# Kernel tuning notes

Hardware: AMD Instinct MI355X
Metric: run time of the kernel (lower is better)

Reference implementation:

```python
import jax, jax.numpy as jnp
import numpy as np

N_NODES = 50000
N_PAIRS = 200000
HID1 = 256
HID2 = 32


def gcn_conv(x, src, dst, W, b, n):
    # PyG GCNConv: project, add self-loops, sym-normalize, scatter-add to dst.
    sl = jnp.arange(n, dtype=src.dtype)
    s = jnp.concatenate([src, sl])
    d = jnp.concatenate([dst, sl])
    deg = jnp.zeros((n,), x.dtype).at[d].add(1.0)
    dinv = jax.lax.rsqrt(deg)  # deg >= 1 due to self-loops
    xw = x @ W  # [n, out]
    msg = xw[s] * (dinv[s] * dinv[d])[:, None]  # [E+n, out]
    out = jax.ops.segment_sum(msg, d, num_segments=n)
    return out + b


def setup_inputs() -> dict:
    key = jax.random.key(0)
    ks = jax.random.split(key, 16)
    inp = {
        "x": jax.random.randint(ks[0], (N_NODES,), 0, N_NODES),
        "edge1": jax.random.randint(ks[1], (2, 1600000), 0, N_NODES),
        "pos": jax.random.randint(ks[2], (N_PAIRS, 2), 0, N_NODES),
        "idx": jax.random.randint(ks[3], (N_PAIRS,), 0, N_PAIRS),
        "ei2": jax.random.randint(ks[4], (2, 1600000), 0, N_PAIRS),
        "emb_table": jax.random.normal(ks[5], (N_NODES + 1, HID1), jnp.float32) * 0.02,
        "W1": jax.random.normal(ks[6], (HID1, HID2), jnp.float32) * (1.0 / np.sqrt(HID1)),
        "b1": jnp.zeros((HID2,), jnp.float32),
        "W2a": jax.random.normal(ks[7], (HID2, HID2), jnp.float32) * (1.0 / np.sqrt(HID2)),
        "b2a": jnp.zeros((HID2,), jnp.float32),
        "W2b": jax.random.normal(ks[8], (HID2, HID2), jnp.float32) * (1.0 / np.sqrt(HID2)),
        "b2b": jnp.zeros((HID2,), jnp.float32),
        "Wp": jax.random.normal(ks[9], (HID2, 1), jnp.float32) * (1.0 / np.sqrt(HID2)),
        "bp": jnp.zeros((1,), jnp.float32),
    }
    return inp


def reference(x, edge1, pos, idx, ei2, emb_table, W1, b1, W2a, b2a, W2b, b2b, Wp, bp):
    # eval mode: all Dropouts are identity; no LayerNorm/GraphNorm (default flags False)
    h = emb_table[x]  # [N, HID1] embedding lookup (squeeze is no-op for 1D ids)
    # conv1s: single GCNConv HID1 -> HID2 + ReLU
    h = jax.nn.relu(gcn_conv(h, edge1[0], edge1[1], W1, b1, N_NODES))
    # pairwise gather-multiply over pos
    h = h[pos[:, 0]] * h[pos[:, 1]]  # [M, HID2]
    # conv2s / conv2s_r on the pair graph (edge2 = ei2, edge2_r = flipped)
    h = (jax.nn.relu(gcn_conv(h, ei2[0], ei2[1], W2a, b2a, N_PAIRS))
         + jax.nn.relu(gcn_conv(h, ei2[1], ei2[0], W2b, b2b, N_PAIRS)))
    # gather by idx, then multiply consecutive (even, odd) rows
    h = h[idx]  # [2Q, HID2]
    h = h[0::2] * h[1::2]  # [Q, HID2]
    return h @ Wp + bp  # [Q, 1]
```

## Files before the change

kernel.cpp:

```cpp
#include <hip/hip_runtime.h>
#include <hip/hip_fp16.h>
#include <math.h>


#define SL     256
#define SLOG   8
#define CAP1   8960
#define CAP2   2432
#define SHIFT1 17
#define SHIFT2 18
#define BCH    8192
#define BT     1024
#define EPT    8
#define MAXSL2 1024
#define PB     64
#define EROW   264

typedef short bf16x8 __attribute__((ext_vector_type(8)));
typedef float f32x4 __attribute__((ext_vector_type(4)));

static __device__ __forceinline__ unsigned short f2bf(float f) {
    union { float f; unsigned u; } v;
    v.f = f;
    unsigned r = v.u + 0x7FFF + ((v.u >> 16) & 1);
    return (unsigned short)(r >> 16);
}
static __device__ __forceinline__ float bf2f(unsigned short h) {
    return __uint_as_float(((unsigned)h) << 16);
}
static __device__ __forceinline__ float bflo(unsigned u) { return __uint_as_float(u << 16); }
static __device__ __forceinline__ float bfhi(unsigned u) { return __uint_as_float(u & 0xFFFF0000u); }

static __device__ __forceinline__ float4 bfacc(float4 a, uint2 w) {
    a.x += bflo(w.x);
    a.y += bfhi(w.x);
    a.z += bflo(w.y);
    a.w += bfhi(w.y);
    return a;
}
static __device__ __forceinline__ float4 hacc(float4 a, uint2 w) {
    float2 f0 = __half22float2(*(__half2*)&w.x);
    float2 f1 = __half22float2(*(__half2*)&w.y);
    a.x += f0.x;
    a.y += f0.y;
    a.z += f1.x;
    a.w += f1.y;
    return a;
}
static __device__ __forceinline__ float4 h2f4(uint2 w) {
    float2 f0 = __half22float2(*(__half2*)&w.x);
    float2 f1 = __half22float2(*(__half2*)&w.y);
    float4 r = {f0.x, f0.y, f1.x, f1.y};
    return r;
}
static __device__ __forceinline__ uint2 f42h(float4 f) {
    __half2 h0 = __floats2half2_rn(f.x, f.y);
    __half2 h1 = __floats2half2_rn(f.z, f.w);
    uint2 r = {*(unsigned*)&h0, *(unsigned*)&h1};
    return r;
}

__global__ __launch_bounds__(256) void k_init(int* __restrict__ bumpF,
                                              int* __restrict__ bumpR,
                                              int* __restrict__ bump1,
                                              int NS2, int NS1) {
    int i = blockIdx.x * 256 + threadIdx.x;
    if (i < NS2) {
        bumpF[i] = i * CAP2;
        bumpR[i] = i * CAP2;
    }
    if (i < NS1) bump1[i] = i * CAP1;
}

__global__ __launch_bounds__(BT) void k_build(const int* __restrict__ s2,
                                              const int* __restrict__ d2,
                                              const int* __restrict__ s1,
                                              const int* __restrict__ d1,
                                              int* bumpF, int* bumpR, int* bump1,
                                              int* __restrict__ bktF,
                                              int* __restrict__ bktR,
                                              int* __restrict__ bkt1,
                                              const float* __restrict__ W1,
                                              const float* __restrict__ W2a,
                                              const float* __restrict__ W2b,
                                              unsigned short* __restrict__ Wbhi,
                                              unsigned short* __restrict__ Wblo,
                                              unsigned short* __restrict__ W2ah,
                                              unsigned short* __restrict__ W2al,
                                              unsigned short* __restrict__ W2bh,
                                              unsigned short* __restrict__ W2bl,
                                              int E2, int E1, int NS2, int NS1,
                                              int NB2, int NB1) {
    __shared__ int stag[BCH];
    __shared__ int lbF[MAXSL2 + 1];
    __shared__ int lbR[MAXSL2 + 1];
    __shared__ int bgF[MAXSL2], bgR[MAXSL2];
    __shared__ int wsum[BT / 64];
    int tid = threadIdx.x, bid = blockIdx.x;
    int lane = tid & 63, wid = tid >> 6;

    auto exscan = [&](int v) -> int {
        int sc = v;
#pragma unroll
        for (int d = 1; d < 64; d <<= 1) {
            int t = __shfl_up(sc, d, 64);
            if (lane >= d) sc += t;
        }
        if (lane == 63) wsum[wid] = sc;
        __syncthreads();
        int woff = 0;
        for (int w2 = 0; w2 < wid; w2++) woff += wsum[w2];
        __syncthreads();
        return woff + sc - v;
    };

    if (bid < NB2) {
        if (tid < NS2) { lbF[tid] = 0; lbR[tid] = 0; }
        __syncthreads();
        int eb = bid * BCH;
        int n = E2 - eb; if (n > BCH) n = BCH;
        int sv[EPT], dv[EPT], ofF[EPT], ofR[EPT];
#pragma unroll
        for (int k = 0; k < EPT; k++) {
            int i = k * BT + tid;
            if (i < n) {
                sv[k] = s2[eb + i];
                dv[k] = d2[eb + i];
                ofF[k] = atomicAdd(&lbF[dv[k] >> SLOG], 1);
                ofR[k] = atomicAdd(&lbR[sv[k] >> SLOG], 1);
            }
        }
        __syncthreads();
        int cF = (tid < NS2) ? lbF[tid] : 0;
        int cR = (tid < NS2) ? lbR[tid] : 0;
        int preF = exscan(cF);
        int preR = exscan(cR);
        if (tid < NS2) {
            lbF[tid] = preF;
            lbR[tid] = preR;
            if (tid == NS2 - 1) {
                lbF[NS2] = preF + cF;
                lbR[NS2] = preR + cR;
            }
            bgF[tid] = cF ? atomicAdd(&bumpF[tid], cF) : 0;
            bgR[tid] = cR ? atomicAdd(&bumpR[tid], cR) : 0;
        }
        __syncthreads();
#pragma unroll
        for (int k = 0; k < EPT; k++) {
            int i = k * BT + tid;
            if (i < n) {
                int sf = dv[k] >> SLOG;
                stag[lbF[sf] + ofF[k]] = ((dv[k] & (SL - 1)) << SHIFT2) | sv[k];
            }
        }
        __syncthreads();
        for (int i = tid; i < n; i += BT) {
            int lo = 0, hi = NS2;
            while (hi - lo > 1) {
                int mid = (lo + hi) >> 1;
                if (lbF[mid] <= i) lo = mid; else hi = mid;
            }
            int gp = bgF[lo] + (i - lbF[lo]);
            if (gp < (lo + 1) * CAP2) bktF[gp] = stag[i];
        }
        __syncthreads();
#pragma unroll
        for (int k = 0; k < EPT; k++) {
            int i = k * BT + tid;
            if (i < n) {
                int sr = sv[k] >> SLOG;
                stag[lbR[sr] + ofR[k]] = ((sv[k] & (SL - 1)) << SHIFT2) | dv[k];
            }
        }
        __syncthreads();
        for (int i = tid; i < n; i += BT) {
            int lo = 0, hi = NS2;
            while (hi - lo > 1) {
                int mid = (lo + hi) >> 1;
                if (lbR[mid] <= i) lo = mid; else hi = mid;
            }
            int gp = bgR[lo] + (i - lbR[lo]);
            if (gp < (lo + 1) * CAP2) bktR[gp] = stag[i];
        }
    } else if (bid < NB2 + NB1) {
        if (tid < NS1) lbF[tid] = 0;
        __syncthreads();
        int eb = (bid - NB2) * BCH;
        int n = E1 - eb; if (n > BCH) n = BCH;
        int sv[EPT], dv[EPT], of[EPT];
#pragma unroll
        for (int k = 0; k < EPT; k++) {
            int i = k * BT + tid;
            if (i < n) {
                sv[k] = s1[eb + i];
                dv[k] = d1[eb + i];
                of[k] = atomicAdd(&lbF[dv[k] >> SLOG], 1);
            }
        }
        __syncthreads();
        int c = (tid < NS1) ? lbF[tid] : 0;
        int pre = exscan(c);
        if (tid < NS1) {
            lbF[tid] = pre;
            if (tid == NS1 - 1) lbF[NS1] = pre + c;
            bgF[tid] = c ? atomicAdd(&bump1[tid], c) : 0;
        }
        __syncthreads();
#pragma unroll
        for (int k = 0; k < EPT; k++) {
            int i = k * BT + tid;
            if (i < n) {
                int sf = dv[k] >> SLOG;
                stag[lbF[sf] + of[k]] = ((dv[k] & (SL - 1)) << SHIFT1) | sv[k];
            }
        }
        __syncthreads();
        for (int i = tid; i < n; i += BT) {
            int lo = 0, hi = NS1;
            while (hi - lo > 1) {
                int mid = (lo + hi) >> 1;
                if (lbF[mid] <= i) lo = mid; else hi = mid;
            }
            int gp = bgF[lo] + (i - lbF[lo]);
            if (gp < (lo + 1) * CAP1) bkt1[gp] = stag[i];
        }
    } else {
        int i = (bid - NB2 - NB1) * BT + tid;
        if (i < 8192) {
            int k = i >> 5, c = i & 31;
            float w = W1[i];
            unsigned short hi = f2bf(w);
            unsigned short lo = f2bf(w - bf2f(hi));
            Wbhi[c * 256 + k] = hi;
            Wblo[c * 256 + k] = lo;
        }
        if (i < 1024) {
            int k = i >> 5, c = i & 31;
            float wa = W2a[i], wb = W2b[i];
            unsigned short ha = f2bf(wa);
            unsigned short hb = f2bf(wb);
            W2ah[c * 32 + k] = ha;
            W2al[c * 32 + k] = f2bf(wa - bf2f(ha));
            W2bh[c * 32 + k] = hb;
            W2bl[c * 32 + k] = f2bf(wb - bf2f(hb));
        }
    }
}

__global__ __launch_bounds__(256) void k_sort2(int* __restrict__ bktF, const int* __restrict__ bumpF,
                                               float* __restrict__ dinvF, int* __restrict__ begF,
                                               int* __restrict__ cntF,
                                               int* __restrict__ bktR, const int* __restrict__ bumpR,
                                               float* __restrict__ dinvR, int* __restrict__ begR,
                                               int* __restrict__ cntR,
                                               int NS2, int NP) {
    __shared__ int sorted[CAP2];
    __shared__ int hist[SL], cursor[SL];
    __shared__ int wsum[4];
    int bid = blockIdx.x;
    int s;
    int* bkt;
    const int* bump;
    float* dinv;
    int* beg;
    int* cntA;
    if (bid < NS2) {
        s = bid;
        bkt = bktF; bump = bumpF; dinv = dinvF; beg = begF; cntA = cntF;
    } else {
        s = bid - NS2;
        bkt = bktR; bump = bumpR; dinv = dinvR; beg = begR; cntA = cntR;
    }
    int tid = threadIdx.x;
    hist[tid] = 0;
    __syncthreads();
    int cnt = bump[s] - s * CAP2;
    if (cnt > CAP2) cnt = CAP2;
    int* b = bkt + (size_t)s * CAP2;
    for (int i = tid; i < cnt; i += 256) atomicAdd(&hist[b[i] >> SHIFT2], 1);
    __syncthreads();
    int c = hist[tid];
    int sc = c;
    int lane = tid & 63, wid = tid >> 6;
#pragma unroll
    for (int d = 1; d < 64; d <<= 1) {
        int t = __shfl_up(sc, d, 64);
        if (lane >= d) sc += t;
    }
    if (lane == 63) wsum[wid] = sc;
    __syncthreads();
    int woff = 0;
    for (int w = 0; w < wid; w++) woff += wsum[w];
    int pre = woff + sc - c;
    cursor[tid] = pre;
    int v = s * SL + tid;
    if (v < NP) {
        dinv[v] = 1.f / sqrtf((float)c + 1.f);
        beg[v] = s * CAP2 + pre;
        cntA[v] = c;
    }
    __syncthreads();
    for (int i = tid; i < cnt; i += 256) {
        int pair = b[i];
        int dl = pair >> SHIFT2;
        int p = atomicAdd(&cursor[dl], 1);
        sorted[p] = pair & ((1 << SHIFT2) - 1);
    }
    __syncthreads();
    for (int i = tid; i < cnt; i += 256) b[i] = sorted[i];
}

__global__ __launch_bounds__(1024) void k_sort1(int* __restrict__ bkt1, const int* __restrict__ bump1,
                                                float* __restrict__ dinv1, int* __restrict__ beg1,
                                                int* __restrict__ cnt1, int N1) {
    __shared__ int sorted[CAP1];
    __shared__ int hist[SL], cursor[SL];
    __shared__ int wsum[4];
    int tid = threadIdx.x, s = blockIdx.x;
    if (tid < SL) hist[tid] = 0;
    __syncthreads();
    int cnt = bump1[s] - s * CAP1;
    if (cnt > CAP1) cnt = CAP1;
    int* b = bkt1 + (size_t)s * CAP1;
    for (int i = tid; i < cnt; i += 1024) atomicAdd(&hist[b[i] >> SHIFT1], 1);
    __syncthreads();
    int c = 0, sc = 0;
    int lane = tid & 63, wid = tid >> 6;
    if (tid < SL) {
        c = hist[tid];
        sc = c;
#pragma unroll
        for (int d = 1; d < 64; d <<= 1) {
            int t = __shfl_up(sc, d, 64);
            if (lane >= d) sc += t;
        }
        if (lane == 63) wsum[wid] = sc;
    }
    __syncthreads();
    if (tid < SL) {
        int woff = 0;
        for (int w = 0; w < wid; w++) woff += wsum[w];
        int pre = woff + sc - c;
        cursor[tid] = pre;
        int v = s * SL + tid;
        if (v < N1) {
            dinv1[v] = 1.f / sqrtf((float)c + 1.f);
            beg1[v] = s * CAP1 + pre;
            cnt1[v] = c;
        }
    }
    __syncthreads();
    for (int i = tid; i < cnt; i += 1024) {
        int pair = b[i];
        int dl = pair >> SHIFT1;
        int p = atomicAdd(&cursor[dl], 1);
        sorted[p] = pair & ((1 << SHIFT1) - 1);
    }
    __syncthreads();
    for (int i = tid; i < cnt; i += 1024) b[i] = sorted[i];
}

__global__ __launch_bounds__(256) void k_xw1(const int* __restrict__ x,
                                             const float* __restrict__ emb,
                                             const unsigned short* __restrict__ Wbhi,
                                             const unsigned short* __restrict__ Wblo,
                                             const float* __restrict__ dinv1,
                                             __half* __restrict__ y1, int N) {
    __shared__ unsigned short sEhi[32 * EROW];
    __shared__ unsigned short sElo[32 * EROW];
    int tid = threadIdx.x;
    int lane = tid & 63, wv = tid >> 6;
    int r0 = blockIdx.x * 32;
    const float4* emb4 = (const float4*)emb;
#pragma unroll
    for (int p = 0; p < 8; p++) {
        int row = p * 4 + wv;
        int r = r0 + row;
        int xr = x[(r < N) ? r : 0];
        float4 e = emb4[(size_t)xr * 64 + lane];
        unsigned short h0 = f2bf(e.x), h1 = f2bf(e.y), h2 = f2bf(e.z), h3 = f2bf(e.w);
        ushort4 hi = {h0, h1, h2, h3};
        ushort4 lo = {f2bf(e.x - bf2f(h0)), f2bf(e.y - bf2f(h1)),
                      f2bf(e.z - bf2f(h2)), f2bf(e.w - bf2f(h3))};
        *(ushort4*)&sEhi[row * EROW + lane * 4] = hi;
        *(ushort4*)&sElo[row * EROW + lane * 4] = lo;
    }
    __syncthreads();
    int col = lane & 15, quad = lane >> 4;
    int rowtile = wv >> 1, ntile = wv & 1;
    f32x4 acc = {0.f, 0.f, 0.f, 0.f};
    const unsigned short* arow_hi = &sEhi[(rowtile * 16 + col) * EROW + quad * 8];
    const unsigned short* arow_lo = &sElo[(rowtile * 16 + col) * EROW + quad * 8];
    const unsigned short* bh = Wbhi + (ntile * 16 + col) * 256 + quad * 8;
    const unsigned short* bl = Wblo + (ntile * 16 + col) * 256 + quad * 8;
#pragma unroll
    for (int kb = 0; kb < 256; kb += 32) {
        bf16x8 ahi = *(const bf16x8*)(arow_hi + kb);
        bf16x8 alo = *(const bf16x8*)(arow_lo + kb);
        bf16x8 bhv = *(const bf16x8*)(bh + kb);
        bf16x8 blv = *(const bf16x8*)(bl + kb);
        acc = __builtin_amdgcn_mfma_f32_16x16x32_bf16(ahi, bhv, acc, 0, 0, 0);
        acc = __builtin_amdgcn_mfma_f32_16x16x32_bf16(alo, bhv, acc, 0, 0, 0);
        acc = __builtin_amdgcn_mfma_f32_16x16x32_bf16(ahi, blv, acc, 0, 0, 0);
    }
#pragma unroll
    for (int reg = 0; reg < 4; reg++) {
        int grow = r0 + rowtile * 16 + quad * 4 + reg;
        if (grow < N) {
            float dv = dinv1[grow];
            y1[grow * 32 + ntile * 16 + col] = __float2half(acc[reg] * dv);
        }
    }
}

static __device__ __forceinline__ float4 gcn_sum_h(const int* __restrict__ adj, int bg, int end,
                                                   const uint2* __restrict__ y2, int q,
                                                   float4 acc) {
    float4 a1 = {0.f, 0.f, 0.f, 0.f};
    int i = bg;
    for (; i + 4 <= end; i += 4) {
        int u0 = adj[i], u1 = adj[i + 1], u2 = adj[i + 2], u3 = adj[i + 3];
        uint2 w0 = y2[u0 * 8 + q];
        uint2 w1 = y2[u1 * 8 + q];
        uint2 w2 = y2[u2 * 8 + q];
        uint2 w3 = y2[u3 * 8 + q];
        acc = hacc(acc, w0);
        a1 = hacc(a1, w1);
        acc = hacc(acc, w2);
        a1 = hacc(a1, w3);
    }
    for (; i < end; i++) acc = hacc(acc, y2[adj[i] * 8 + q]);
    acc.x += a1.x;
    acc.y += a1.y;
    acc.z += a1.z;
    acc.w += a1.w;
    return acc;
}

static __device__ __forceinline__ float4 gcn_sum_bf(const int* __restrict__ adj, int bg, int end,
                                                    const uint2* __restrict__ y2, int q,
                                                    float4 acc) {
    float4 a1 = {0.f, 0.f, 0.f, 0.f};
    int i = bg;
    for (; i + 4 <= end; i += 4) {
        int u0 = adj[i], u1 = adj[i + 1], u2 = adj[i + 2], u3 = adj[i + 3];
        uint2 w0 = y2[u0 * 8 + q];
        uint2 w1 = y2[u1 * 8 + q];
        uint2 w2 = y2[u2 * 8 + q];
        uint2 w3 = y2[u3 * 8 + q];
        acc = bfacc(acc, w0);
        a1 = bfacc(a1, w1);
        acc = bfacc(acc, w2);
        a1 = bfacc(a1, w3);
    }
    for (; i < end; i++) acc = bfacc(acc, y2[adj[i] * 8 + q]);
    acc.x += a1.x;
    acc.y += a1.y;
    acc.z += a1.z;
    acc.w += a1.w;
    return acc;
}

__global__ __launch_bounds__(256) void k_gath1(const int* __restrict__ adj,
                                               const int* __restrict__ beg,
                                               const int* __restrict__ cntA,
                                               const float* __restrict__ dinv,
                                               const __half* __restrict__ y1,
                                               __half* __restrict__ out1, int N) {
    int gid = blockIdx.x * 256 + threadIdx.x;
    int v = gid >> 3, q = gid & 7;
    if (v >= N) return;
    int bg = beg[v];
    int end = bg + cntA[v];
    float dv = dinv[v];
    const uint2* y2 = (const uint2*)y1;
    float4 acc = {0.f, 0.f, 0.f, 0.f};
    acc = hacc(acc, y2[v * 8 + q]);
    acc = gcn_sum_h(adj, bg, end, y2, q, acc);
    acc.x *= dv;
    acc.y *= dv;
    acc.z *= dv;
    acc.w *= dv;
    ((uint2*)out1)[v * 8 + q] = f42h(acc);
}

__global__ __launch_bounds__(256) void k_gathF(const int* __restrict__ adjF,
                                               const int* __restrict__ begF,
                                               const int* __restrict__ cntF,
                                               const float* __restrict__ dinvF,
                                               const unsigned short* __restrict__ ya,
                                               __half* __restrict__ o2a, int N) {
    int gid = blockIdx.x * 256 + threadIdx.x;
    int v = gid >> 3, q = gid & 7;
    if (v >= N) return;
    float dvF = dinvF[v];
    const uint2* ya2 = (const uint2*)ya;
    float4 aF = {0.f, 0.f, 0.f, 0.f};
    aF = bfacc(aF, ya2[v * 8 + q]);
    int bgF = begF[v];
    aF = gcn_sum_bf(adjF, bgF, bgF + cntF[v], ya2, q, aF);
    aF.x *= dvF;
    aF.y *= dvF;
    aF.z *= dvF;
    aF.w *= dvF;
    ((uint2*)o2a)[v * 8 + q] = f42h(aF);
}

__global__ __launch_bounds__(256) void k_gathR(const int* __restrict__ adjR,
                                               const int* __restrict__ begR,
                                               const int* __restrict__ cntR,
                                               const float* __restrict__ dinvR,
                                               const unsigned short* __restrict__ yb,
                                               const __half* __restrict__ o2a,
                                               const float* __restrict__ b2a,
                                               const float* __restrict__ b2b,
                                               __half* __restrict__ h3, int N) {
    int gid = blockIdx.x * 256 + threadIdx.x;
    int v = gid >> 3, q = gid & 7;
    if (v >= N) return;
    float dvR = dinvR[v];
    const uint2* yb2 = (const uint2*)yb;
    float4 aR = {0.f, 0.f, 0.f, 0.f};
    aR = bfacc(aR, yb2[v * 8 + q]);
    int bgR = begR[v];
    aR = gcn_sum_bf(adjR, bgR, bgR + cntR[v], yb2, q, aR);
    float4 oa = h2f4(((const uint2*)o2a)[v * 8 + q]);
    float4 ba = ((const float4*)b2a)[q];
    float4 bb = ((const float4*)b2b)[q];
    float4 h;
    h.x = fmaxf(oa.x + ba.x, 0.f) + fmaxf(fmaf(aR.x, dvR, bb.x), 0.f);
    h.y = fmaxf(oa.y + ba.y, 0.f) + fmaxf(fmaf(aR.y, dvR, bb.y), 0.f);
    h.z = fmaxf(oa.z + ba.z, 0.f) + fmaxf(fmaf(aR.z, dvR, bb.z), 0.f);
    h.w = fmaxf(oa.w + ba.w, 0.f) + fmaxf(fmaf(aR.w, dvR, bb.w), 0.f);
    ((uint2*)h3)[v * 8 + q] = f42h(h);
}

__global__ __launch_bounds__(256) void k_xw2(const int* __restrict__ pos,
                                             const __half* __restrict__ out1,
                                             const float* __restrict__ b1,
                                             const unsigned short* __restrict__ W2ah,
                                             const unsigned short* __restrict__ W2al,
                                             const unsigned short* __restrict__ W2bh,
                                             const unsigned short* __restrict__ W2bl,
                                             const float* __restrict__ dinvF,
                                             const float* __restrict__ dinvR,
                                             unsigned short* __restrict__ ya,
                                             unsigned short* __restrict__ yb,
                                             int NP) {
    __shared__ unsigned short sHhi[PB * 32];
    __shared__ unsigned short sHlo[PB * 32];
    __shared__ int sPos[PB * 2];
    int tid = threadIdx.x;
    int p0 = blockIdx.x * PB;
    if (tid < PB * 2) {
        int gi = p0 * 2 + tid;
        sPos[tid] = (gi < NP * 2) ? pos[gi] : 0;
    }
    __syncthreads();
    const uint2* o12 = (const uint2*)out1;
    int q = tid & 7;
    float4 bq = ((const float4*)b1)[q];
#pragma unroll
    for (int half = 0; half < 2; half++) {
        int p = half * 32 + (tid >> 3);
        int ra = sPos[2 * p] * 8, rb = sPos[2 * p + 1] * 8;
        float4 ea = h2f4(o12[ra + q]);
        float4 eb = h2f4(o12[rb + q]);
        float4 h;
        h.x = fmaxf(ea.x + bq.x, 0.f) * fmaxf(eb.x + bq.x, 0.f);
        h.y = fmaxf(ea.y + bq.y, 0.f) * fmaxf(eb.y + bq.y, 0.f);
        h.z = fmaxf(ea.z + bq.z, 0.f) * fmaxf(eb.z + bq.z, 0.f);
        h.w = fmaxf(ea.w + bq.w, 0.f) * fmaxf(eb.w + bq.w, 0.f);
        unsigned short h0 = f2bf(h.x), h1 = f2bf(h.y), h2 = f2bf(h.z), h3 = f2bf(h.w);
        ushort4 hi = {h0, h1, h2, h3};
        ushort4 lo = {f2bf(h.x - bf2f(h0)), f2bf(h.y - bf2f(h1)),
                      f2bf(h.z - bf2f(h2)), f2bf(h.w - bf2f(h3))};
        *(ushort4*)&sHhi[p * 32 + q * 4] = hi;
        *(ushort4*)&sHlo[p * 32 + q * 4] = lo;
    }
    __syncthreads();
    int lane = tid & 63, wv = tid >> 6;
    int col = lane & 15, quad = lane >> 4;
    bf16x8 ahi = *(const bf16x8*)&sHhi[(wv * 16 + col) * 32 + quad * 8];
    bf16x8 alo = *(const bf16x8*)&sHlo[(wv * 16 + col) * 32 + quad * 8];
    f32x4 accA[2], accB[2];
#pragma unroll
    for (int nt = 0; nt < 2; nt++) {
        int off = (nt * 16 + col) * 32 + quad * 8;
        bf16x8 bah = *(const bf16x8*)(W2ah + off);
        bf16x8 bal = *(const bf16x8*)(W2al + off);
        bf16x8 bbh = *(const bf16x8*)(W2bh + off);
        bf16x8 bbl = *(const bf16x8*)(W2bl + off);
        f32x4 z = {0.f, 0.f, 0.f, 0.f};
        f32x4 a = __builtin_amdgcn_mfma_f32_16x16x32_bf16(ahi, bah, z, 0, 0, 0);
        a = __builtin_amdgcn_mfma_f32_16x16x32_bf16(alo, bah, a, 0, 0, 0);
        a = __builtin_amdgcn_mfma_f32_16x16x32_bf16(ahi, bal, a, 0, 0, 0);
        accA[nt] = a;
        f32x4 b = __builtin_amdgcn_mfma_f32_16x16x32_bf16(ahi, bbh, z, 0, 0, 0);
        b = __builtin_amdgcn_mfma_f32_16x16x32_bf16(alo, bbh, b, 0, 0, 0);
        b = __builtin_amdgcn_mfma_f32_16x16x32_bf16(ahi, bbl, b, 0, 0, 0);
        accB[nt] = b;
    }
#pragma unroll
    for (int reg = 0; reg < 4; reg++) {
        int p = wv * 16 + quad * 4 + reg;
        int pg = p0 + p;
        if (pg < NP) {
            float dA = dinvF[pg], dB = dinvR[pg];
#pragma unroll
            for (int nt = 0; nt < 2; nt++) {
                ya[pg * 32 + nt * 16 + col] = f2bf(accA[nt][reg] * dA);
                yb[pg * 32 + nt * 16 + col] = f2bf(accB[nt][reg] * dB);
            }
        }
    }
}

__global__ __launch_bounds__(256) void k_final(const int* __restrict__ idx,
                                               const __half* __restrict__ h3,
                                               const float* __restrict__ Wp,
                                               const float* __restrict__ bp,
                                               float* __restrict__ out, int Q) {
    int gid = blockIdx.x * 256 + threadIdx.x;
    int qi = gid >> 3, q = gid & 7;
    if (qi >= Q) return;
    int i0 = idx[2 * qi] * 8, i1 = idx[2 * qi + 1] * 8;
    float4 wp = ((const float4*)Wp)[q];
    const uint2* H = (const uint2*)h3;
    float4 h0 = h2f4(H[i0 + q]), h1 = h2f4(H[i1 + q]);
    float s = h0.x * h1.x * wp.x + h0.y * h1.y * wp.y + h0.z * h1.z * wp.z + h0.w * h1.w * wp.w;
    s += __shfl_xor(s, 1);
    s += __shfl_xor(s, 2);
    s += __shfl_xor(s, 4);
    if (q == 0) out[qi] = s + bp[0];
}

extern "C" void kernel_launch(void* const* d_in, const int* in_sizes, int n_in,
                              void* d_out, int out_size, void* d_ws, size_t ws_size,
                              hipStream_t stream) {
    const int* x    = (const int*)d_in[0];
    const int* e1   = (const int*)d_in[1];
    const int* pos  = (const int*)d_in[2];
    const int* idx  = (const int*)d_in[3];
    const int* e2   = (const int*)d_in[4];
    const float* emb = (const float*)d_in[5];
    const float* W1  = (const float*)d_in[6];
    const float* b1  = (const float*)d_in[7];
    const float* W2a = (const float*)d_in[8];
    const float* b2a = (const float*)d_in[9];
    const float* W2b = (const float*)d_in[10];
    const float* b2b = (const float*)d_in[11];
    const float* Wp  = (const float*)d_in[12];
    const float* bp  = (const float*)d_in[13];

    const int N1 = in_sizes[0];
    const int E1 = in_sizes[1] / 2;
    const int NP = in_sizes[3];
    const int E2 = in_sizes[4] / 2;
    const int Q  = out_size;
    (void)n_in; (void)ws_size;

    const int NS1 = (N1 + SL - 1) >> SLOG;
    const int NS2 = (NP + SL - 1) >> SLOG;

    char* w = (char*)d_ws;
    size_t o = 0;
    auto alloc = [&](size_t bytes) { size_t r = o; o += (bytes + 255) & ~(size_t)255; return r; };
    float* dinv1  = (float*)(w + alloc((size_t)(N1 + 2 * NP) * 4));
    float* dinv2f = dinv1 + N1;
    float* dinv2r = dinv2f + NP;
    int* beg1  = (int*)(w + alloc((size_t)(N1 + 2 * NP) * 4));
    int* beg2f = beg1 + N1;
    int* beg2r = beg2f + NP;
    int* cnt1  = (int*)(w + alloc((size_t)(N1 + 2 * NP) * 4));
    int* cnt2f = cnt1 + N1;
    int* cnt2r = cnt2f + NP;
    int* bumpF = (int*)(w + alloc((size_t)(2 * NS2 + NS1) * 4));
    int* bumpR = bumpF + NS2;
    int* bump1 = bumpR + NS2;
    unsigned short* Wbhi = (unsigned short*)(w + alloc(8192 * 2));
    unsigned short* Wblo = (unsigned short*)(w + alloc(8192 * 2));
    unsigned short* W2ah = (unsigned short*)(w + alloc(1024 * 2));
    unsigned short* W2al = (unsigned short*)(w + alloc(1024 * 2));
    unsigned short* W2bh = (unsigned short*)(w + alloc(1024 * 2));
    unsigned short* W2bl = (unsigned short*)(w + alloc(1024 * 2));
    int* bktF = (int*)(w + alloc((size_t)NS2 * CAP2 * 4));
    int* bktR = (int*)(w + alloc((size_t)NS2 * CAP2 * 4));
    int* bkt1 = (int*)(w + alloc((size_t)NS1 * CAP1 * 4));
    __half* out1 = (__half*)(w + alloc((size_t)N1 * 32 * 2));
    __half* y1   = (__half*)(w + alloc((size_t)N1 * 32 * 2));
    unsigned short* ya = (unsigned short*)(w + alloc((size_t)NP * 32 * 2));
    unsigned short* yb = (unsigned short*)(w + alloc((size_t)NP * 32 * 2));
    __half* o2a = (__half*)(w + alloc((size_t)NP * 32 * 2));
    __half* h3  = (__half*)(w + alloc((size_t)NP * 32 * 2));

    const int B = 256;
    auto cdiv = [](long long a, long long b) { return (int)((a + b - 1) / b); };
    const int NB2 = cdiv(E2, BCH), NB1 = cdiv(E1, BCH);
    const int NBW = cdiv(8192, BT);

    k_init<<<cdiv(NS2 > NS1 ? NS2 : NS1, B), B, 0, stream>>>(bumpF, bumpR, bump1, NS2, NS1);
    k_build<<<NB2 + NB1 + NBW, BT, 0, stream>>>(e2, e2 + E2, e1, e1 + E1,
                                                bumpF, bumpR, bump1, bktF, bktR, bkt1,
                                                W1, W2a, W2b, Wbhi, Wblo,
                                                W2ah, W2al, W2bh, W2bl,
                                                E2, E1, NS2, NS1, NB2, NB1);
    k_sort1<<<NS1, 1024, 0, stream>>>(bkt1, bump1, dinv1, beg1, cnt1, N1);
    k_sort2<<<2 * NS2, B, 0, stream>>>(bktF, bumpF, dinv2f, beg2f, cnt2f,
                                       bktR, bumpR, dinv2r, beg2r, cnt2r, NS2, NP);
    k_xw1<<<cdiv(N1, 32), B, 0, stream>>>(x, emb, Wbhi, Wblo, dinv1, y1, N1);
    k_gath1<<<cdiv((long long)N1 * 8, B), B, 0, stream>>>(bkt1, beg1, cnt1, dinv1, y1, out1, N1);
    k_xw2<<<cdiv(NP, PB), B, 0, stream>>>(pos, out1, b1, W2ah, W2al, W2bh, W2bl,
                                          dinv2f, dinv2r, ya, yb, NP);
    k_gathF<<<cdiv((long long)NP * 8, B), B, 0, stream>>>(bktF, beg2f, cnt2f, dinv2f, ya, o2a, NP);
    k_gathR<<<cdiv((long long)NP * 8, B), B, 0, stream>>>(bktR, beg2r, cnt2r, dinv2r, yb,
                                                          o2a, b2a, b2b, h3, NP);
    k_final<<<cdiv((long long)Q * 8, B), B, 0, stream>>>(idx, h3, Wp, bp, (float*)d_out, Q);
}
```

Baseline: 295.1 us.

## Shrink first-graph buckets, merge sort kernels, fuse forward/reverse pair gathers

The first graph's bucket width drops from 256 to 64 nodes so it can share the 256-thread sort kernel with the pair graph, merging two sort launches into one. The build kernel now stores each staged edge's bucket id in a short shared array, replacing the per-element binary search over bucket offsets. The separate forward and reverse pair-graph gather kernels are fused into one, removing the o2a intermediate round trip through global memory. In exchange there are more buckets for graph 1 (more global atomics and sort blocks), extra shared memory in build, and higher per-thread work in the fused gather.

```diff
diff --git a/kernel.cpp b/kernel.cpp
--- a/kernel.cpp
+++ b/kernel.cpp
@@ -5,10 +5,10 @@
 
 #define SL     256
 #define SLOG   8
-#define CAP1   8960
-#define CAP2   2432
-#define SHIFT1 17
-#define SHIFT2 18
+#define SL1    64
+#define SLOG1  6
+#define CAP    2432
+#define SHIFT  18
 #define BCH    8192
 #define BT     1024
 #define EPT    8
@@ -66,10 +66,10 @@
                                               int NS2, int NS1) {
     int i = blockIdx.x * 256 + threadIdx.x;
     if (i < NS2) {
-        bumpF[i] = i * CAP2;
-        bumpR[i] = i * CAP2;
-    }
-    if (i < NS1) bump1[i] = i * CAP1;
+        bumpF[i] = i * CAP;
+        bumpR[i] = i * CAP;
+    }
+    if (i < NS1) bump1[i] = i * CAP;
 }
 
 __global__ __launch_bounds__(BT) void k_build(const int* __restrict__ s2,
@@ -92,8 +92,9 @@
                                               int E2, int E1, int NS2, int NS1,
                                               int NB2, int NB1) {
     __shared__ int stag[BCH];
-    __shared__ int lbF[MAXSL2 + 1];
-    __shared__ int lbR[MAXSL2 + 1];
+    __shared__ unsigned short stag2[BCH];
+    __shared__ int lbF[MAXSL2];
+    __shared__ int lbR[MAXSL2];
     __shared__ int bgF[MAXSL2], bgR[MAXSL2];
     __shared__ int wsum[BT / 64];
     int tid = threadIdx.x, bid = blockIdx.x;
@@ -138,10 +139,6 @@
         if (tid < NS2) {
             lbF[tid] = preF;
             lbR[tid] = preR;
-            if (tid == NS2 - 1) {
-                lbF[NS2] = preF + cF;
-                lbR[NS2] = preR + cR;
-            }
             bgF[tid] = cF ? atomicAdd(&bumpF[tid], cF) : 0;
             bgR[tid] = cR ? atomicAdd(&bumpR[tid], cR) : 0;
         }
@@ -151,18 +148,16 @@
             int i = k * BT + tid;
             if (i < n) {
                 int sf = dv[k] >> SLOG;
-                stag[lbF[sf] + ofF[k]] = ((dv[k] & (SL - 1)) << SHIFT2) | sv[k];
+                int p = lbF[sf] + ofF[k];
+                stag[p] = ((dv[k] & (SL - 1)) << SHIFT) | sv[k];
+                stag2[p] = (unsigned short)sf;
             }
         }
         __syncthreads();
         for (int i = tid; i < n; i += BT) {
-            int lo = 0, hi = NS2;
-            while (hi - lo > 1) {
-                int mid = (lo + hi) >> 1;
-                if (lbF[mid] <= i) lo = mid; else hi = mid;
-            }
-            int gp = bgF[lo] + (i - lbF[lo]);
-            if (gp < (lo + 1) * CAP2) bktF[gp] = stag[i];
+            int sf = stag2[i];
+            int gp = bgF[sf] + (i - lbF[sf]);
+            if (gp < (sf + 1) * CAP) bktF[gp] = stag[i];
         }
         __syncthreads();
 #pragma unroll
@@ -170,18 +165,16 @@
             int i = k * BT + tid;
             if (i < n) {
                 int sr = sv[k] >> SLOG;
-                stag[lbR[sr] + ofR[k]] = ((sv[k] & (SL - 1)) << SHIFT2) | dv[k];
+                int p = lbR[sr] + ofR[k];
+                stag[p] = ((sv[k] & (SL - 1)) << SHIFT) | dv[k];
+                stag2[p] = (unsigned short)sr;
             }
         }
         __syncthreads();
         for (int i = tid; i < n; i += BT) {
-            int lo = 0, hi = NS2;
-            while (hi - lo > 1) {
-                int mid = (lo + hi) >> 1;
-                if (lbR[mid] <= i) lo = mid; else hi = mid;
-            }
-            int gp = bgR[lo] + (i - lbR[lo]);
-            if (gp < (lo + 1) * CAP2) bktR[gp] = stag[i];
+            int sr = stag2[i];
+            int gp = bgR[sr] + (i - lbR[sr]);
+            if (gp < (sr + 1) * CAP) bktR[gp] = stag[i];
         }
     } else if (bid < NB2 + NB1) {
         if (tid < NS1) lbF[tid] = 0;
@@ -195,7 +188,7 @@
             if (i < n) {
                 sv[k] = s1[eb + i];
                 dv[k] = d1[eb + i];
-                of[k] = atomicAdd(&lbF[dv[k] >> SLOG], 1);
+                of[k] = atomicAdd(&lbF[dv[k] >> SLOG1], 1);
             }
         }
         __syncthreads();
@@ -203,7 +196,6 @@
         int pre = exscan(c);
         if (tid < NS1) {
             lbF[tid] = pre;
-            if (tid == NS1 - 1) lbF[NS1] = pre + c;
             bgF[tid] = c ? atomicAdd(&bump1[tid], c) : 0;
         }
         __syncthreads();
@@ -211,19 +203,17 @@
         for (int k = 0; k < EPT; k++) {
             int i = k * BT + tid;
             if (i < n) {
-                int sf = dv[k] >> SLOG;
-                stag[lbF[sf] + of[k]] = ((dv[k] & (SL - 1)) << SHIFT1) | sv[k];
+                int sf = dv[k] >> SLOG1;
+                int p = lbF[sf] + of[k];
+                stag[p] = ((dv[k] & (SL1 - 1)) << SHIFT) | sv[k];
+                stag2[p] = (unsigned short)sf;
             }
         }
         __syncthreads();
         for (int i = tid; i < n; i += BT) {
-            int lo = 0, hi = NS1;
-            while (hi - lo > 1) {
-                int mid = (lo + hi) >> 1;
-                if (lbF[mid] <= i) lo = mid; else hi = mid;
-            }
-            int gp = bgF[lo] + (i - lbF[lo]);
-            if (gp < (lo + 1) * CAP1) bkt1[gp] = stag[i];
+            int sf = stag2[i];
+            int gp = bgF[sf] + (i - lbF[sf]);
+            if (gp < (sf + 1) * CAP) bkt1[gp] = stag[i];
         }
     } else {
         int i = (bid - NB2 - NB1) * BT + tid;
@@ -248,39 +238,47 @@
     }
 }
 
-__global__ __launch_bounds__(256) void k_sort2(int* __restrict__ bktF, const int* __restrict__ bumpF,
-                                               float* __restrict__ dinvF, int* __restrict__ begF,
-                                               int* __restrict__ cntF,
-                                               int* __restrict__ bktR, const int* __restrict__ bumpR,
-                                               float* __restrict__ dinvR, int* __restrict__ begR,
-                                               int* __restrict__ cntR,
-                                               int NS2, int NP) {
-    __shared__ int sorted[CAP2];
+__global__ __launch_bounds__(256) void k_sort(int* __restrict__ bkt1, const int* __restrict__ bump1,
+                                              float* __restrict__ dinv1, int* __restrict__ beg1,
+                                              int* __restrict__ cnt1,
+                                              int* __restrict__ bktF, const int* __restrict__ bumpF,
+                                              float* __restrict__ dinvF, int* __restrict__ begF,
+                                              int* __restrict__ cntF,
+                                              int* __restrict__ bktR, const int* __restrict__ bumpR,
+                                              float* __restrict__ dinvR, int* __restrict__ begR,
+                                              int* __restrict__ cntR,
+                                              int NS1, int NS2, int N1, int NP) {
+    __shared__ int sorted[CAP];
     __shared__ int hist[SL], cursor[SL];
     __shared__ int wsum[4];
-    int bid = blockIdx.x;
-    int s;
+    int bid = blockIdx.x, tid = threadIdx.x;
+    int s, sls, N;
     int* bkt;
     const int* bump;
     float* dinv;
     int* beg;
     int* cntA;
-    if (bid < NS2) {
+    if (bid < NS1) {
         s = bid;
+        bkt = bkt1; bump = bump1; dinv = dinv1; beg = beg1; cntA = cnt1;
+        sls = SL1; N = N1;
+    } else if (bid < NS1 + NS2) {
+        s = bid - NS1;
         bkt = bktF; bump = bumpF; dinv = dinvF; beg = begF; cntA = cntF;
+        sls = SL; N = NP;
     } else {
-        s = bid - NS2;
+        s = bid - NS1 - NS2;
         bkt = bktR; bump = bumpR; dinv = dinvR; beg = begR; cntA = cntR;
-    }
-    int tid = threadIdx.x;
+        sls = SL; N = NP;
+    }
     hist[tid] = 0;
     __syncthreads();
-    int cnt = bump[s] - s * CAP2;
-    if (cnt > CAP2) cnt = CAP2;
-    int* b = bkt + (size_t)s * CAP2;
-    for (int i = tid; i < cnt; i += 256) atomicAdd(&hist[b[i] >> SHIFT2], 1);
-    __syncthreads();
-    int c = hist[tid];
+    int cnt = bump[s] - s * CAP;
+    if (cnt > CAP) cnt = CAP;
+    int* b = bkt + (size_t)s * CAP;
+    for (int i = tid; i < cnt; i += 256) atomicAdd(&hist[b[i] >> SHIFT], 1);
+    __syncthreads();
+    int c = (tid < sls) ? hist[tid] : 0;
     int sc = c;
     int lane = tid & 63, wid = tid >> 6;
 #pragma unroll
@@ -294,71 +292,23 @@
     for (int w = 0; w < wid; w++) woff += wsum[w];
     int pre = woff + sc - c;
     cursor[tid] = pre;
-    int v = s * SL + tid;
-    if (v < NP) {
-        dinv[v] = 1.f / sqrtf((float)c + 1.f);
-        beg[v] = s * CAP2 + pre;
-        cntA[v] = c;
+    if (tid < sls) {
+        int v = s * sls + tid;
+        if (v < N) {
+            dinv[v] = 1.f / sqrtf((float)c + 1.f);
+            beg[v] = s * CAP + pre;
+            cntA[v] = c;
+        }
     }
     __syncthreads();
     for (int i = tid; i < cnt; i += 256) {
         int pair = b[i];
-        int dl = pair >> SHIFT2;
+        int dl = pair >> SHIFT;
         int p = atomicAdd(&cursor[dl], 1);
-        sorted[p] = pair & ((1 << SHIFT2) - 1);
+        sorted[p] = pair & ((1 << SHIFT) - 1);
     }
     __syncthreads();
     for (int i = tid; i < cnt; i += 256) b[i] = sorted[i];
-}
-
-__global__ __launch_bounds__(1024) void k_sort1(int* __restrict__ bkt1, const int* __restrict__ bump1,
-                                                float* __restrict__ dinv1, int* __restrict__ beg1,
-                                                int* __restrict__ cnt1, int N1) {
-    __shared__ int sorted[CAP1];
-    __shared__ int hist[SL], cursor[SL];
-    __shared__ int wsum[4];
-    int tid = threadIdx.x, s = blockIdx.x;
-    if (tid < SL) hist[tid] = 0;
-    __syncthreads();
-    int cnt = bump1[s] - s * CAP1;
-    if (cnt > CAP1) cnt = CAP1;
-    int* b = bkt1 + (size_t)s * CAP1;
-    for (int i = tid; i < cnt; i += 1024) atomicAdd(&hist[b[i] >> SHIFT1], 1);
-    __syncthreads();
-    int c = 0, sc = 0;
-    int lane = tid & 63, wid = tid >> 6;
-    if (tid < SL) {
-        c = hist[tid];
-        sc = c;
-#pragma unroll
-        for (int d = 1; d < 64; d <<= 1) {
-            int t = __shfl_up(sc, d, 64);
-            if (lane >= d) sc += t;
-        }
-        if (lane == 63) wsum[wid] = sc;
-    }
-    __syncthreads();
-    if (tid < SL) {
-        int woff = 0;
-        for (int w = 0; w < wid; w++) woff += wsum[w];
-        int pre = woff + sc - c;
-        cursor[tid] = pre;
-        int v = s * SL + tid;
-        if (v < N1) {
-            dinv1[v] = 1.f / sqrtf((float)c + 1.f);
-            beg1[v] = s * CAP1 + pre;
-            cnt1[v] = c;
-        }
-    }
-    __syncthreads();
-    for (int i = tid; i < cnt; i += 1024) {
-        int pair = b[i];
-        int dl = pair >> SHIFT1;
-        int p = atomicAdd(&cursor[dl], 1);
-        sorted[p] = pair & ((1 << SHIFT1) - 1);
-    }
-    __syncthreads();
-    for (int i = tid; i < cnt; i += 1024) b[i] = sorted[i];
 }
 
 __global__ __launch_bounds__(256) void k_xw1(const int* __restrict__ x,
@@ -485,54 +435,40 @@
     ((uint2*)out1)[v * 8 + q] = f42h(acc);
 }
 
-__global__ __launch_bounds__(256) void k_gathF(const int* __restrict__ adjF,
+__global__ __launch_bounds__(256) void k_gath2(const int* __restrict__ adjF,
                                                const int* __restrict__ begF,
                                                const int* __restrict__ cntF,
                                                const float* __restrict__ dinvF,
                                                const unsigned short* __restrict__ ya,
-                                               __half* __restrict__ o2a, int N) {
-    int gid = blockIdx.x * 256 + threadIdx.x;
-    int v = gid >> 3, q = gid & 7;
-    if (v >= N) return;
-    float dvF = dinvF[v];
-    const uint2* ya2 = (const uint2*)ya;
-    float4 aF = {0.f, 0.f, 0.f, 0.f};
-    aF = bfacc(aF, ya2[v * 8 + q]);
-    int bgF = begF[v];
-    aF = gcn_sum_bf(adjF, bgF, bgF + cntF[v], ya2, q, aF);
-    aF.x *= dvF;
-    aF.y *= dvF;
-    aF.z *= dvF;
-    aF.w *= dvF;
-    ((uint2*)o2a)[v * 8 + q] = f42h(aF);
-}
-
-__global__ __launch_bounds__(256) void k_gathR(const int* __restrict__ adjR,
+                                               const int* __restrict__ adjR,
                                                const int* __restrict__ begR,
                                                const int* __restrict__ cntR,
                                                const float* __restrict__ dinvR,
                                                const unsigned short* __restrict__ yb,
-                                               const __half* __restrict__ o2a,
                                                const float* __restrict__ b2a,
                                                const float* __restrict__ b2b,
                                                __half* __restrict__ h3, int N) {
     int gid = blockIdx.x * 256 + threadIdx.x;
     int v = gid >> 3, q = gid & 7;
     if (v >= N) return;
-    float dvR = dinvR[v];
+    const uint2* ya2 = (const uint2*)ya;
     const uint2* yb2 = (const uint2*)yb;
+    float4 aF = {0.f, 0.f, 0.f, 0.f};
+    aF = bfacc(aF, ya2[v * 8 + q]);
+    int bF = begF[v];
+    aF = gcn_sum_bf(adjF, bF, bF + cntF[v], ya2, q, aF);
     float4 aR = {0.f, 0.f, 0.f, 0.f};
     aR = bfacc(aR, yb2[v * 8 + q]);
-    int bgR = begR[v];
-    aR = gcn_sum_bf(adjR, bgR, bgR + cntR[v], yb2, q, aR);
-    float4 oa = h2f4(((const uint2*)o2a)[v * 8 + q]);
+    int bR = begR[v];
+    aR = gcn_sum_bf(adjR, bR, bR + cntR[v], yb2, q, aR);
+    float dvF = dinvF[v], dvR = dinvR[v];
     float4 ba = ((const float4*)b2a)[q];
     float4 bb = ((const float4*)b2b)[q];
     float4 h;
-    h.x = fmaxf(oa.x + ba.x, 0.f) + fmaxf(fmaf(aR.x, dvR, bb.x), 0.f);
-    h.y = fmaxf(oa.y + ba.y, 0.f) + fmaxf(fmaf(aR.y, dvR, bb.y), 0.f);
-    h.z = fmaxf(oa.z + ba.z, 0.f) + fmaxf(fmaf(aR.z, dvR, bb.z), 0.f);
-    h.w = fmaxf(oa.w + ba.w, 0.f) + fmaxf(fmaf(aR.w, dvR, bb.w), 0.f);
+    h.x = fmaxf(fmaf(aF.x, dvF, ba.x), 0.f) + fmaxf(fmaf(aR.x, dvR, bb.x), 0.f);
+    h.y = fmaxf(fmaf(aF.y, dvF, ba.y), 0.f) + fmaxf(fmaf(aR.y, dvR, bb.y), 0.f);
+    h.z = fmaxf(fmaf(aF.z, dvF, ba.z), 0.f) + fmaxf(fmaf(aR.z, dvR, bb.z), 0.f);
+    h.w = fmaxf(fmaf(aF.w, dvF, ba.w), 0.f) + fmaxf(fmaf(aR.w, dvR, bb.w), 0.f);
     ((uint2*)h3)[v * 8 + q] = f42h(h);
 }
 
@@ -661,7 +597,7 @@
     const int Q  = out_size;
     (void)n_in; (void)ws_size;
 
-    const int NS1 = (N1 + SL - 1) >> SLOG;
+    const int NS1 = (N1 + SL1 - 1) >> SLOG1;
     const int NS2 = (NP + SL - 1) >> SLOG;
 
     char* w = (char*)d_ws;
@@ -685,14 +621,13 @@
     unsigned short* W2al = (unsigned short*)(w + alloc(1024 * 2));
     unsigned short* W2bh = (unsigned short*)(w + alloc(1024 * 2));
     unsigned short* W2bl = (unsigned short*)(w + alloc(1024 * 2));
-    int* bktF = (int*)(w + alloc((size_t)NS2 * CAP2 * 4));
-    int* bktR = (int*)(w + alloc((size_t)NS2 * CAP2 * 4));
-    int* bkt1 = (int*)(w + alloc((size_t)NS1 * CAP1 * 4));
+    int* bktF = (int*)(w + alloc((size_t)NS2 * CAP * 4));
+    int* bktR = (int*)(w + alloc((size_t)NS2 * CAP * 4));
+    int* bkt1 = (int*)(w + alloc((size_t)NS1 * CAP * 4));
     __half* out1 = (__half*)(w + alloc((size_t)N1 * 32 * 2));
     __half* y1   = (__half*)(w + alloc((size_t)N1 * 32 * 2));
     unsigned short* ya = (unsigned short*)(w + alloc((size_t)NP * 32 * 2));
     unsigned short* yb = (unsigned short*)(w + alloc((size_t)NP * 32 * 2));
-    __half* o2a = (__half*)(w + alloc((size_t)NP * 32 * 2));
     __half* h3  = (__half*)(w + alloc((size_t)NP * 32 * 2));
 
     const int B = 256;
@@ -706,15 +641,16 @@
                                                 W1, W2a, W2b, Wbhi, Wblo,
                                                 W2ah, W2al, W2bh, W2bl,
                                                 E2, E1, NS2, NS1, NB2, NB1);
-    k_sort1<<<NS1, 1024, 0, stream>>>(bkt1, bump1, dinv1, beg1, cnt1, N1);
-    k_sort2<<<2 * NS2, B, 0, stream>>>(bktF, bumpF, dinv2f, beg2f, cnt2f,
-                                       bktR, bumpR, dinv2r, beg2r, cnt2r, NS2, NP);
+    k_sort<<<NS1 + 2 * NS2, B, 0, stream>>>(bkt1, bump1, dinv1, beg1, cnt1,
+                                            bktF, bumpF, dinv2f, beg2f, cnt2f,
+                                            bktR, bumpR, dinv2r, beg2r, cnt2r,
+                                            NS1, NS2, N1, NP);
     k_xw1<<<cdiv(N1, 32), B, 0, stream>>>(x, emb, Wbhi, Wblo, dinv1, y1, N1);
     k_gath1<<<cdiv((long long)N1 * 8, B), B, 0, stream>>>(bkt1, beg1, cnt1, dinv1, y1, out1, N1);
     k_xw2<<<cdiv(NP, PB), B, 0, stream>>>(pos, out1, b1, W2ah, W2al, W2bh, W2bl,
                                           dinv2f, dinv2r, ya, yb, NP);
-    k_gathF<<<cdiv((long long)NP * 8, B), B, 0, stream>>>(bktF, beg2f, cnt2f, dinv2f, ya, o2a, NP);
-    k_gathR<<<cdiv((long long)NP * 8, B), B, 0, stream>>>(bktR, beg2r, cnt2r, dinv2r, yb,
-                                                          o2a, b2a, b2b, h3, NP);
+    k_gath2<<<cdiv((long long)NP * 8, B), B, 0, stream>>>(bktF, beg2f, cnt2f, dinv2f, ya,
+                                                          bktR, beg2r, cnt2r, dinv2r, yb,
+                                                          b2a, b2b, h3, NP);
     k_final<<<cdiv((long long)Q * 8, B), B, 0, stream>>>(idx, h3, Wp, bp, (float*)d_out, Q);
 }
```

New measurement: 281.0 us. 1.05x faster.
